# Kernel optimization log

Measured on AMD Instinct MI355X. Metric: run time of the kernel, lower is better.

## Reference

```python
import jax, jax.numpy as jnp
import numpy as np

D = 2048
H = 16
DH = D // H
L = 512  # kv_latent_dim
LN_EPS = 1e-5


def setup_inputs() -> dict:
    key = jax.random.key(0)
    ks = jax.random.split(key, 8)
    s = 0.02  # weight init scale to keep logits in a sane range
    x = jax.random.normal(ks[0], (2, 2048, D), dtype=jnp.float32)
    W_q = jax.random.normal(ks[1], (D, D), dtype=jnp.float32) * s      # torch Linear weight [out,in]
    Wd_kv = jax.random.normal(ks[2], (L, D), dtype=jnp.float32) * s
    W_uv = jax.random.normal(ks[3], (D, L), dtype=jnp.float32) * s
    W_uk = jax.random.normal(ks[4], (D, L), dtype=jnp.float32) * s
    W_o = jax.random.normal(ks[5], (D, D), dtype=jnp.float32) * s
    gamma = jnp.ones((L,), dtype=jnp.float32)
    beta = jnp.zeros((L,), dtype=jnp.float32)
    return {"x": x, "W_q": W_q, "Wd_kv": Wd_kv, "W_uv": W_uv, "W_uk": W_uk,
            "W_o": W_o, "gamma": gamma, "beta": beta}


def _layernorm(h, gamma, beta):
    mu = jnp.mean(h, axis=-1, keepdims=True)
    var = jnp.mean(jnp.square(h - mu), axis=-1, keepdims=True)
    return (h - mu) * jax.lax.rsqrt(var + LN_EPS) * gamma + beta


def reference(x, W_q, Wd_kv, W_uv, W_uk, W_o, gamma, beta):
    B, S, _ = x.shape
    # absorbed K projection: (W_q @ W_uk) -> [H, dh, L]
    absorbed_k = (W_q @ W_uk).reshape(H, DH, L)
    # latent KV: layernorm(x @ Wd_kv^T), [B, S, L]
    c_kv = _layernorm(jnp.einsum('bsd,ld->bsl', x, Wd_kv), gamma, beta)
    S_full = c_kv.shape[1]
    # NOTE: original uses raw x (not W_q(x)) as q; W_q is folded into absorbed_k
    q = x.reshape(B, S, H, DH)
    tmp = jnp.einsum('bshd,hdl->bhsl', q, absorbed_k)              # [B,H,S,L]
    scores = jnp.einsum('bhsl,btl->bhst', tmp, c_kv) / np.sqrt(DH)  # [B,H,S,S_full]
    # causal mask (past_length=0)
    mask = jnp.tril(jnp.ones((S, S_full), dtype=bool), k=0)
    scores = jnp.where(mask[None, None], scores, -jnp.inf)
    attn = jax.nn.softmax(scores, axis=-1)
    v_full = jnp.einsum('btl,dl->btd', c_kv, W_uv).reshape(B, S_full, H, DH)
    ctx = jnp.einsum('bhst,bthd->bshd', attn, v_full).reshape(B, S, D)
    out = jnp.einsum('bsd,od->bso', ctx, W_o)
    return out, c_kv
```

## Files before the change

### kernel.cpp

```cpp
#include <hip/hip_runtime.h>
#include <hip/hip_bf16.h>
#include <cstdint>


typedef __bf16 bf16x8 __attribute__((ext_vector_type(8)));
typedef __bf16 bf16x4 __attribute__((ext_vector_type(4)));
typedef float  f32x4  __attribute__((ext_vector_type(4)));

#define GLOBAL_AS __attribute__((address_space(1)))
#define LDS_AS    __attribute__((address_space(3)))

__device__ __forceinline__ void gload_lds16(const void* g, void* l) {
    __builtin_amdgcn_global_load_lds((const GLOBAL_AS uint32_t*)g,
                                     (LDS_AS uint32_t*)l, 16, 0, 0);
}

__global__ void k_prep(const float* __restrict__ x, const float* __restrict__ wq,
                       const float* __restrict__ wdkv, const float* __restrict__ wuv,
                       const float* __restrict__ wo, const float* __restrict__ wuk,
                       __bf16* __restrict__ xb, __bf16* __restrict__ wqb,
                       __bf16* __restrict__ wdkvb, __bf16* __restrict__ wuvb,
                       __bf16* __restrict__ wob, __bf16* __restrict__ wukT) {
    __shared__ float t[64][65];
    const int bidx = blockIdx.x;
    if (bidx < 9216) {
        long i = (long)bidx * blockDim.x + threadIdx.x;
        const float* src; __bf16* dst; long off;
        if (i < 1048576)      { src = x;    dst = xb;    off = i; }
        else if (i < 1572864) { src = wq;   dst = wqb;   off = i - 1048576; }
        else if (i < 1703936) { src = wdkv; dst = wdkvb; off = i - 1572864; }
        else if (i < 1835008) { src = wuv;  dst = wuvb;  off = i - 1703936; }
        else                  { src = wo;   dst = wob;   off = i - 1835008; }
        long e = off * 8;
        float4 a = *reinterpret_cast<const float4*>(src + e);
        float4 b = *reinterpret_cast<const float4*>(src + e + 4);
        bf16x8 r;
        r[0] = (__bf16)a.x; r[1] = (__bf16)a.y; r[2] = (__bf16)a.z; r[3] = (__bf16)a.w;
        r[4] = (__bf16)b.x; r[5] = (__bf16)b.y; r[6] = (__bf16)b.z; r[7] = (__bf16)b.w;
        *reinterpret_cast<bf16x8*>(dst + e) = r;
    } else {
        const int tb = bidx - 9216;
        const int d0 = (tb & 31) * 64, l0 = (tb >> 5) * 64;
        const int tid = threadIdx.x;
        const int r = tid >> 4, c = (tid & 15) * 4;
        #pragma unroll
        for (int rr = 0; rr < 64; rr += 16) {
            float4 v = *reinterpret_cast<const float4*>(&wuk[(long)(d0 + r + rr) * 512 + l0 + c]);
            t[r + rr][c] = v.x; t[r + rr][c + 1] = v.y;
            t[r + rr][c + 2] = v.z; t[r + rr][c + 3] = v.w;
        }
        __syncthreads();
        const int lr = tid >> 2, dc = (tid & 3) * 16;
        bf16x8 o0, o1;
        #pragma unroll
        for (int i = 0; i < 8; ++i) { o0[i] = (__bf16)t[dc + i][lr]; o1[i] = (__bf16)t[dc + 8 + i][lr]; }
        *reinterpret_cast<bf16x8*>(&wukT[(long)(l0 + lr) * 2048 + d0 + dc]) = o0;
        *reinterpret_cast<bf16x8*>(&wukT[(long)(l0 + lr) * 2048 + d0 + dc + 8]) = o1;
    }
}

__global__ __launch_bounds__(256, 2) void k_gemm_g12(
    const __bf16* __restrict__ Wqb, const __bf16* __restrict__ WukT, __bf16* __restrict__ absk,
    const __bf16* __restrict__ xb, const __bf16* __restrict__ Wdkvb, float* __restrict__ ckvpre,
    float cscale)
{
    __shared__ __bf16 Asm[128][64];
    __shared__ __bf16 Bsm[64][64];
    const int bid = blockIdx.x;
    const bool g1s = (bid < 128);
    const int lbid = g1s ? bid : bid - 128;
    const int tm = (lbid >> 3) * 128, tn = (lbid & 7) * 64;
    const __bf16* A = g1s ? Wqb : xb;
    const __bf16* B = g1s ? WukT : Wdkvb;
    const int tid  = threadIdx.x;
    const int lane = tid & 63, wid = tid >> 6;
    const int r16 = lane & 15, g = lane >> 4;
    const int srow  = lane >> 3;
    const int sslot = lane & 7;
    const int scol  = ((sslot ^ srow) * 8);

    f32x4 acc[2][4];
    #pragma unroll
    for (int m = 0; m < 2; ++m)
        #pragma unroll
        for (int n = 0; n < 4; ++n) acc[m][n] = (f32x4){0.f, 0.f, 0.f, 0.f};

    for (int kt = 0; kt < 2048; kt += 64) {
        __syncthreads();
        #pragma unroll
        for (int c2 = 0; c2 < 4; ++c2) {
            const int chunk = wid * 4 + c2;
            const int row   = chunk * 8 + srow;
            gload_lds16(&A[(long)(tm + row) * 2048 + kt + scol], &Asm[chunk * 8][0]);
        }
        #pragma unroll
        for (int c2 = 0; c2 < 2; ++c2) {
            const int chunk = wid * 2 + c2;
            const int row   = chunk * 8 + srow;
            gload_lds16(&B[(long)(tn + row) * 2048 + kt + scol], &Bsm[chunk * 8][0]);
        }
        __syncthreads();
        #pragma unroll
        for (int kk = 0; kk < 2; ++kk) {
            bf16x8 af[2], bfr[4];
            #pragma unroll
            for (int m = 0; m < 2; ++m) {
                const int row = wid * 32 + m * 16 + r16;
                af[m] = *reinterpret_cast<const bf16x8*>(
                    reinterpret_cast<const char*>(&Asm[0][0]) +
                    row * 128 + (((kk * 4 + g) ^ (row & 7)) * 16));
            }
            #pragma unroll
            for (int n = 0; n < 4; ++n) {
                const int row = n * 16 + r16;
                bfr[n] = *reinterpret_cast<const bf16x8*>(
                    reinterpret_cast<const char*>(&Bsm[0][0]) +
                    row * 128 + (((kk * 4 + g) ^ (row & 7)) * 16));
            }
            #pragma unroll
            for (int m = 0; m < 2; ++m)
                #pragma unroll
                for (int n = 0; n < 4; ++n)
                    acc[m][n] = __builtin_amdgcn_mfma_f32_16x16x32_bf16(af[m], bfr[n], acc[m][n], 0, 0, 0);
        }
    }
    #pragma unroll
    for (int m = 0; m < 2; ++m) {
        #pragma unroll
        for (int n = 0; n < 4; ++n) {
            #pragma unroll
            for (int j = 0; j < 4; ++j) {
                const int row = tm + wid * 32 + m * 16 + g * 4 + j;
                const int col = tn + n * 16 + r16;
                if (g1s) absk[(long)row * 512 + col] = (__bf16)(acc[m][n][j] * cscale);
                else     ckvpre[(long)row * 512 + col] = acc[m][n][j];
            }
        }
    }
}

template <typename CT>
__global__ __launch_bounds__(256, 2) void k_gemm_bt(
    const __bf16* __restrict__ A, const __bf16* __restrict__ B, CT* __restrict__ C,
    int K, int lda, int ldb, int ldc,
    long aOffZ, long bOffZ, long cOffZ, float cmul)
{
    A += (long)blockIdx.z * aOffZ;
    B += (long)blockIdx.z * bOffZ;
    C += (long)blockIdx.z * cOffZ;
    __shared__ __bf16 Asm[128][64];
    __shared__ __bf16 Bsm[128][64];
    const int tid  = threadIdx.x;
    const int lane = tid & 63, wid = tid >> 6;
    const int wr = wid >> 1, wc = wid & 1;
    const int tm = blockIdx.x * 128, tn = blockIdx.y * 128;
    const int r16 = lane & 15, g = lane >> 4;

    const int srow  = lane >> 3;
    const int sslot = lane & 7;
    const int scol  = ((sslot ^ srow) * 8);

    f32x4 acc[4][4];
    #pragma unroll
    for (int m = 0; m < 4; ++m)
        #pragma unroll
        for (int n = 0; n < 4; ++n) acc[m][n] = (f32x4){0.f, 0.f, 0.f, 0.f};

    for (int kt = 0; kt < K; kt += 64) {
        __syncthreads();
        #pragma unroll
        for (int c2 = 0; c2 < 4; ++c2) {
            const int chunk = wid * 4 + c2;
            const int row   = chunk * 8 + srow;
            gload_lds16(&A[(long)(tm + row) * lda + kt + scol], &Asm[chunk * 8][0]);
            gload_lds16(&B[(long)(tn + row) * ldb + kt + scol], &Bsm[chunk * 8][0]);
        }
        __syncthreads();
        #pragma unroll
        for (int kk = 0; kk < 2; ++kk) {
            bf16x8 af[4], bfr[4];
            #pragma unroll
            for (int m = 0; m < 4; ++m) {
                const int row = wr * 64 + m * 16 + r16;
                af[m] = *reinterpret_cast<const bf16x8*>(
                    reinterpret_cast<const char*>(&Asm[0][0]) +
                    row * 128 + (((kk * 4 + g) ^ (row & 7)) * 16));
            }
            #pragma unroll
            for (int n = 0; n < 4; ++n) {
                const int row = wc * 64 + n * 16 + r16;
                bfr[n] = *reinterpret_cast<const bf16x8*>(
                    reinterpret_cast<const char*>(&Bsm[0][0]) +
                    row * 128 + (((kk * 4 + g) ^ (row & 7)) * 16));
            }
            #pragma unroll
            for (int m = 0; m < 4; ++m)
                #pragma unroll
                for (int n = 0; n < 4; ++n)
                    acc[m][n] = __builtin_amdgcn_mfma_f32_16x16x32_bf16(af[m], bfr[n], acc[m][n], 0, 0, 0);
        }
    }
    #pragma unroll
    for (int m = 0; m < 4; ++m) {
        #pragma unroll
        for (int n = 0; n < 4; ++n) {
            #pragma unroll
            for (int j = 0; j < 4; ++j) {
                const int row = tm + wr * 64 + m * 16 + g * 4 + j;
                const int col = tn + wc * 64 + n * 16 + r16;
                C[(long)row * ldc + col] = (CT)(acc[m][n][j] * cmul);
            }
        }
    }
}

__global__ void k_layernorm(const float* __restrict__ pre, const float* __restrict__ gamma,
                            const float* __restrict__ beta, float* __restrict__ out_f32,
                            __bf16* __restrict__ out_bf16) {
    const int row  = blockIdx.x * 4 + (threadIdx.x >> 6);
    const int lane = threadIdx.x & 63;
    const float* p = pre + (long)row * 512;
    float4 v0 = *reinterpret_cast<const float4*>(p + lane * 4);
    float4 v1 = *reinterpret_cast<const float4*>(p + 256 + lane * 4);
    float s  = v0.x + v0.y + v0.z + v0.w + v1.x + v1.y + v1.z + v1.w;
    float s2 = v0.x*v0.x + v0.y*v0.y + v0.z*v0.z + v0.w*v0.w
             + v1.x*v1.x + v1.y*v1.y + v1.z*v1.z + v1.w*v1.w;
    #pragma unroll
    for (int d = 1; d < 64; d <<= 1) { s += __shfl_xor(s, d); s2 += __shfl_xor(s2, d); }
    const float mu  = s * (1.0f / 512.0f);
    const float var = s2 * (1.0f / 512.0f) - mu * mu;
    const float rs  = rsqrtf(var + 1e-5f);
    float4 g0 = *reinterpret_cast<const float4*>(gamma + lane * 4);
    float4 g1 = *reinterpret_cast<const float4*>(gamma + 256 + lane * 4);
    float4 b0 = *reinterpret_cast<const float4*>(beta + lane * 4);
    float4 b1 = *reinterpret_cast<const float4*>(beta + 256 + lane * 4);
    float4 y0, y1;
    y0.x = (v0.x - mu) * rs * g0.x + b0.x;  y0.y = (v0.y - mu) * rs * g0.y + b0.y;
    y0.z = (v0.z - mu) * rs * g0.z + b0.z;  y0.w = (v0.w - mu) * rs * g0.w + b0.w;
    y1.x = (v1.x - mu) * rs * g1.x + b1.x;  y1.y = (v1.y - mu) * rs * g1.y + b1.y;
    y1.z = (v1.z - mu) * rs * g1.z + b1.z;  y1.w = (v1.w - mu) * rs * g1.w + b1.w;
    *reinterpret_cast<float4*>(out_f32 + (long)row * 512 + lane * 4) = y0;
    *reinterpret_cast<float4*>(out_f32 + (long)row * 512 + 256 + lane * 4) = y1;
    bf16x4 z0, z1;
    z0[0] = (__bf16)y0.x; z0[1] = (__bf16)y0.y; z0[2] = (__bf16)y0.z; z0[3] = (__bf16)y0.w;
    z1[0] = (__bf16)y1.x; z1[1] = (__bf16)y1.y; z1[2] = (__bf16)y1.z; z1[3] = (__bf16)y1.w;
    *reinterpret_cast<bf16x4*>(out_bf16 + (long)row * 512 + lane * 4) = z0;
    *reinterpret_cast<bf16x4*>(out_bf16 + (long)row * 512 + 256 + lane * 4) = z1;
}

__global__ __launch_bounds__(256, 2) void k_attn(
    const __bf16* __restrict__ xb,
    const __bf16* __restrict__ Keff,
    const __bf16* __restrict__ vT,
    __bf16* __restrict__ ctx)
{
    __shared__ __bf16 Ks[2][64][128];
    __shared__ __bf16 Vs[2][128][64];
    __shared__ __bf16 Pl[4][16][72];
    const int lane = threadIdx.x & 63;
    const int wid  = threadIdx.x >> 6;
    const int r16  = lane & 15;
    const int g    = lane >> 4;
    const int bid  = blockIdx.x;
    const int gidx = ((bid >> 7) << 3) | (bid & 7);
    const int h = gidx & 15, b = gidx >> 4;
    const int p = (bid >> 3) & 15;
    const int nkt = 32 - p;
    const int qbase[2] = { p * 64 + wid * 16, (31 - p) * 64 + wid * 16 };

    bf16x8 aQ[2][4];
    #pragma unroll
    for (int st = 0; st < 2; ++st) {
        const __bf16* qp = xb + ((long)(b * 2048 + qbase[st] + r16)) * 2048 + h * 128 + g * 8;
        #pragma unroll
        for (int ks = 0; ks < 4; ++ks)
            aQ[st][ks] = *reinterpret_cast<const bf16x8*>(qp + ks * 32);
    }

    f32x4 o[2][8];
    float mrow[2], lrow[2];
    #pragma unroll
    for (int st = 0; st < 2; ++st) {
        #pragma unroll
        for (int d8 = 0; d8 < 8; ++d8) o[st][d8] = (f32x4){0.f, 0.f, 0.f, 0.f};
        mrow[st] = -__builtin_inff(); lrow[st] = 0.f;
    }

    const __bf16* Kb = Keff + (long)h * (4096 * 128) + (long)b * (2048 * 128);
    const __bf16* Vb = vT + (long)h * (128 * 4096) + b * 2048;

    const int ksrow = wid * 4 + (lane >> 4);
    const int kslot = lane & 15;
    const int vsrow = wid * 8 + (lane >> 3);
    const int vslot = lane & 7;

    auto stage = [&](int kt, int buf) {
        const int k0s = kt * 64;
        #pragma unroll
        for (int c = 0; c < 4; ++c) {
            const int row = c * 16 + ksrow;
            const int gcol = ((kslot ^ (row & 15)) << 3);
            gload_lds16(&Kb[(long)(k0s + row) * 128 + gcol], &Ks[buf][c * 16 + wid * 4][0]);
        }
        #pragma unroll
        for (int c = 0; c < 4; ++c) {
            const int row = c * 32 + vsrow;
            const int gcol = ((vslot ^ (row & 7)) << 3);
            gload_lds16(&Vb[(long)row * 4096 + k0s + gcol], &Vs[buf][c * 32 + wid * 8][0]);
        }
    };

    const float THR = 11.541560327f;
    stage(0, 0);
    for (int kt = 0; kt < nkt; ++kt) {
        const int cur = kt & 1;
        const int k0 = kt * 64;
        __syncthreads();
        if (kt + 1 < nkt) stage(kt + 1, cur ^ 1);
        const char* Kbase = reinterpret_cast<const char*>(&Ks[cur][0][0]);
        const char* Vbase = reinterpret_cast<const char*>(&Vs[cur][0][0]);
        const bool light = (kt <= p);

        f32x4 sT[2][4];
        #pragma unroll
        for (int kh = 0; kh < 4; ++kh) {
            sT[0][kh] = (f32x4){0.f, 0.f, 0.f, 0.f};
            sT[1][kh] = (f32x4){0.f, 0.f, 0.f, 0.f};
        }
        __builtin_amdgcn_s_setprio(1);
        #pragma unroll
        for (int kh = 0; kh < 4; ++kh) {
            const int krow = kh * 16 + r16;
            bf16x8 bk[4];
            #pragma unroll
            for (int ks = 0; ks < 4; ++ks)
                bk[ks] = *reinterpret_cast<const bf16x8*>(
                    Kbase + krow * 256 + (((ks * 4 + g) ^ (krow & 15)) * 16));
            #pragma unroll
            for (int ks = 0; ks < 4; ++ks)
                sT[1][kh] = __builtin_amdgcn_mfma_f32_16x16x32_bf16(bk[ks], aQ[1][ks], sT[1][kh], 0, 0, 0);
            if (light) {
                #pragma unroll
                for (int ks = 0; ks < 4; ++ks)
                    sT[0][kh] = __builtin_amdgcn_mfma_f32_16x16x32_bf16(bk[ks], aQ[0][ks], sT[0][kh], 0, 0, 0);
            }
        }
        __builtin_amdgcn_s_setprio(0);

        bf16x8 pa[2][2];
        #pragma unroll
        for (int sti = 0; sti < 2; ++sti) {
            const int st = 1 - sti;
            if (st == 0 && !light) continue;
            const bool diag = (st == 0) ? (kt == p) : (kt == nkt - 1);
            if (diag) {
                const int qabs = qbase[st] + r16;
                #pragma unroll
                for (int kh = 0; kh < 4; ++kh)
                    #pragma unroll
                    for (int j = 0; j < 4; ++j)
                        if (k0 + kh * 16 + g * 4 + j > qabs) sT[st][kh][j] = -1e30f;
            }
            float t01 = fmaxf(sT[st][0][0], sT[st][0][1]), t23 = fmaxf(sT[st][0][2], sT[st][0][3]);
            float t45 = fmaxf(sT[st][1][0], sT[st][1][1]), t67 = fmaxf(sT[st][1][2], sT[st][1][3]);
            float t89 = fmaxf(sT[st][2][0], sT[st][2][1]), tab = fmaxf(sT[st][2][2], sT[st][2][3]);
            float tcd = fmaxf(sT[st][3][0], sT[st][3][1]), tef = fmaxf(sT[st][3][2], sT[st][3][3]);
            float tmax = fmaxf(fmaxf(fmaxf(t01, t23), fmaxf(t45, t67)),
                               fmaxf(fmaxf(t89, tab), fmaxf(tcd, tef)));
            tmax = fmaxf(tmax, __shfl_xor(tmax, 16));
            tmax = fmaxf(tmax, __shfl_xor(tmax, 32));
            const int needi = !__all(tmax <= mrow[st] + THR);
            float m = mrow[st], alpha = 1.f;
            if (needi) {
                const float mnew = fmaxf(m, tmax);
                alpha = __builtin_amdgcn_exp2f(m - mnew);
                m = mnew; mrow[st] = mnew;
            }
            float rsum = 0.f;
            bf16x4 pb[4];
            #pragma unroll
            for (int kh = 0; kh < 4; ++kh) {
                #pragma unroll
                for (int j = 0; j < 4; ++j) {
                    const float pv = __builtin_amdgcn_exp2f(sT[st][kh][j] - m);
                    rsum += pv;
                    pb[kh][j] = (__bf16)pv;
                }
            }
            rsum += __shfl_xor(rsum, 16);
            rsum += __shfl_xor(rsum, 32);
            lrow[st] = lrow[st] * alpha + rsum;
            #pragma unroll
            for (int kh = 0; kh < 4; ++kh)
                *reinterpret_cast<bf16x4*>(&Pl[wid][r16][kh * 16 + g * 4]) = pb[kh];
            pa[st][0] = *reinterpret_cast<const bf16x8*>(&Pl[wid][r16][g * 8]);
            pa[st][1] = *reinterpret_cast<const bf16x8*>(&Pl[wid][r16][32 + g * 8]);
            if (needi) {
                float a4[4];
                #pragma unroll
                for (int j = 0; j < 4; ++j) a4[j] = __shfl(alpha, g * 4 + j);
                #pragma unroll
                for (int d8 = 0; d8 < 8; ++d8) {
                    o[st][d8][0] *= a4[0]; o[st][d8][1] *= a4[1];
                    o[st][d8][2] *= a4[2]; o[st][d8][3] *= a4[3];
                }
            }
        }

        __builtin_amdgcn_s_setprio(1);
        #pragma unroll
        for (int kk = 0; kk < 2; ++kk) {
            #pragma unroll
            for (int d8 = 0; d8 < 8; ++d8) {
                const int vrow = d8 * 16 + r16;
                bf16x8 bv = *reinterpret_cast<const bf16x8*>(
                    Vbase + vrow * 128 + (((kk * 4 + g) ^ (vrow & 7)) * 16));
                o[1][d8] = __builtin_amdgcn_mfma_f32_16x16x32_bf16(pa[1][kk], bv, o[1][d8], 0, 0, 0);
                if (light)
                    o[0][d8] = __builtin_amdgcn_mfma_f32_16x16x32_bf16(pa[0][kk], bv, o[0][d8], 0, 0, 0);
            }
        }
        __builtin_amdgcn_s_setprio(0);
    }
    #pragma unroll
    for (int st = 0; st < 2; ++st) {
        float rl4[4];
        #pragma unroll
        for (int j = 0; j < 4; ++j) rl4[j] = 1.0f / __shfl(lrow[st], g * 4 + j);
        #pragma unroll
        for (int d8 = 0; d8 < 8; ++d8) {
            #pragma unroll
            for (int j = 0; j < 4; ++j) {
                const int row = qbase[st] + g * 4 + j;
                ctx[((long)(b * 2048 + row)) * 2048 + h * 128 + d8 * 16 + r16] =
                    (__bf16)(o[st][d8][j] * rl4[j]);
            }
        }
    }
}

extern "C" void kernel_launch(void* const* d_in, const int* in_sizes, int n_in,
                              void* d_out, int out_size, void* d_ws, size_t ws_size,
                              hipStream_t stream) {
    const float* x     = (const float*)d_in[0];
    const float* W_q   = (const float*)d_in[1];
    const float* Wd_kv = (const float*)d_in[2];
    const float* W_uv  = (const float*)d_in[3];
    const float* W_uk  = (const float*)d_in[4];
    const float* W_o   = (const float*)d_in[5];
    const float* gamma = (const float*)d_in[6];
    const float* beta  = (const float*)d_in[7];
    float* out     = (float*)d_out;
    float* ckv_out = out + 8388608;

    char* ws = (char*)d_ws;
    __bf16* xb     = (__bf16*)(ws + 0);
    __bf16* Wqb    = (__bf16*)(ws + 16777216);
    __bf16* Wdkvb  = (__bf16*)(ws + 25165824);
    __bf16* Wuvb   = (__bf16*)(ws + 27262976);
    __bf16* Wob    = (__bf16*)(ws + 29360128);
    __bf16* WukT   = (__bf16*)(ws + 37748736);
    __bf16* absk   = (__bf16*)(ws + 39845888);
    float*  ckvpre = (float*) (ws + 41943040);
    __bf16* ckvb   = (__bf16*)(ws + 50331648);
    __bf16* Keff   = (__bf16*)(ws + 54525952);
    __bf16* vT     = (__bf16*)(ws + 71303168);
    __bf16* ctx    = (__bf16*)(ws + 88080384);

    k_prep<<<9472, 256, 0, stream>>>(x, W_q, Wd_kv, W_uv, W_o, W_uk,
                                     xb, Wqb, Wdkvb, Wuvb, Wob, WukT);

    const float cscale = 1.4426950408889634f * 0.08838834764831845f;
    k_gemm_g12<<<384, 256, 0, stream>>>(Wqb, WukT, absk, xb, Wdkvb, ckvpre, cscale);
    k_layernorm<<<1024, 256, 0, stream>>>(ckvpre, gamma, beta, ckv_out, ckvb);
    k_gemm_bt<__bf16><<<dim3(32, 1, 16), 256, 0, stream>>>(ckvb, absk, Keff,
        512, 512, 512, 128, 0, 128 * 512, 4096 * 128, 1.0f);
    k_gemm_bt<__bf16><<<dim3(16, 32, 1), 256, 0, stream>>>(Wuvb, ckvb, vT,
        512, 512, 512, 4096, 0, 0, 0, 1.0f);
    k_attn<<<512, 256, 0, stream>>>(xb, Keff, vT, ctx);
    k_gemm_bt<float><<<dim3(32, 16, 1), 256, 0, stream>>>(ctx, Wob, out,
        2048, 2048, 2048, 2048, 0, 0, 0, 1.0f);
}
```

Measured before the change: 193.9 us.

## Give each attention wave 32 query rows using two 64-lane waves per block

The attention kernel now runs 2 waves per block instead of 4. Each wave owns two 16-row query groups, so every K and V fragment read from LDS feeds two MFMAs instead of one. The K/V staging loops are re-indexed so the smaller block still fills the same tiles. This cuts LDS read traffic per MFMA, at the cost of doubled accumulator registers and fewer resident waves per CU to hide latency.

```diff
diff --git a/kernel.cpp b/kernel.cpp
--- a/kernel.cpp
+++ b/kernel.cpp
@@ -248,7 +248,7 @@
     *reinterpret_cast<bf16x4*>(out_bf16 + (long)row * 512 + 256 + lane * 4) = z1;
 }
 
-__global__ __launch_bounds__(256, 2) void k_attn(
+__global__ __launch_bounds__(128, 1) void k_attn(
     const __bf16* __restrict__ xb,
     const __bf16* __restrict__ Keff,
     const __bf16* __restrict__ vT,
@@ -256,7 +256,7 @@
 {
     __shared__ __bf16 Ks[2][64][128];
     __shared__ __bf16 Vs[2][128][64];
-    __shared__ __bf16 Pl[4][16][72];
+    __shared__ __bf16 Pl[2][32][72];
     const int lane = threadIdx.x & 63;
     const int wid  = threadIdx.x >> 6;
     const int r16  = lane & 15;
@@ -266,25 +266,29 @@
     const int h = gidx & 15, b = gidx >> 4;
     const int p = (bid >> 3) & 15;
     const int nkt = 32 - p;
-    const int qbase[2] = { p * 64 + wid * 16, (31 - p) * 64 + wid * 16 };
-
-    bf16x8 aQ[2][4];
-    #pragma unroll
-    for (int st = 0; st < 2; ++st) {
-        const __bf16* qp = xb + ((long)(b * 2048 + qbase[st] + r16)) * 2048 + h * 128 + g * 8;
-        #pragma unroll
-        for (int ks = 0; ks < 4; ++ks)
-            aQ[st][ks] = *reinterpret_cast<const bf16x8*>(qp + ks * 32);
-    }
-
-    f32x4 o[2][8];
-    float mrow[2], lrow[2];
-    #pragma unroll
-    for (int st = 0; st < 2; ++st) {
-        #pragma unroll
-        for (int d8 = 0; d8 < 8; ++d8) o[st][d8] = (f32x4){0.f, 0.f, 0.f, 0.f};
-        mrow[st] = -__builtin_inff(); lrow[st] = 0.f;
-    }
+    const int qbase[2] = { p * 64 + wid * 32, (31 - p) * 64 + wid * 32 };
+
+    bf16x8 aQ[2][2][4];
+    #pragma unroll
+    for (int st = 0; st < 2; ++st)
+        #pragma unroll
+        for (int rg = 0; rg < 2; ++rg) {
+            const __bf16* qp = xb + ((long)(b * 2048 + qbase[st] + rg * 16 + r16)) * 2048 + h * 128 + g * 8;
+            #pragma unroll
+            for (int ks = 0; ks < 4; ++ks)
+                aQ[st][rg][ks] = *reinterpret_cast<const bf16x8*>(qp + ks * 32);
+        }
+
+    f32x4 o[2][2][8];
+    float mrow[2][2], lrow[2][2];
+    #pragma unroll
+    for (int st = 0; st < 2; ++st)
+        #pragma unroll
+        for (int rg = 0; rg < 2; ++rg) {
+            #pragma unroll
+            for (int d8 = 0; d8 < 8; ++d8) o[st][rg][d8] = (f32x4){0.f, 0.f, 0.f, 0.f};
+            mrow[st][rg] = -__builtin_inff(); lrow[st][rg] = 0.f;
+        }
 
     const __bf16* Kb = Keff + (long)h * (4096 * 128) + (long)b * (2048 * 128);
     const __bf16* Vb = vT + (long)h * (128 * 4096) + b * 2048;
@@ -297,16 +301,16 @@
     auto stage = [&](int kt, int buf) {
         const int k0s = kt * 64;
         #pragma unroll
-        for (int c = 0; c < 4; ++c) {
-            const int row = c * 16 + ksrow;
+        for (int c = 0; c < 8; ++c) {
+            const int row = c * 8 + ksrow;
             const int gcol = ((kslot ^ (row & 15)) << 3);
-            gload_lds16(&Kb[(long)(k0s + row) * 128 + gcol], &Ks[buf][c * 16 + wid * 4][0]);
-        }
-        #pragma unroll
-        for (int c = 0; c < 4; ++c) {
-            const int row = c * 32 + vsrow;
+            gload_lds16(&Kb[(long)(k0s + row) * 128 + gcol], &Ks[buf][c * 8 + wid * 4][0]);
+        }
+        #pragma unroll
+        for (int c = 0; c < 8; ++c) {
+            const int row = c * 16 + vsrow;
             const int gcol = ((vslot ^ (row & 7)) << 3);
-            gload_lds16(&Vb[(long)row * 4096 + k0s + gcol], &Vs[buf][c * 32 + wid * 8][0]);
+            gload_lds16(&Vb[(long)row * 4096 + k0s + gcol], &Vs[buf][c * 16 + wid * 8][0]);
         }
     };
 
@@ -321,12 +325,13 @@
         const char* Vbase = reinterpret_cast<const char*>(&Vs[cur][0][0]);
         const bool light = (kt <= p);
 
-        f32x4 sT[2][4];
-        #pragma unroll
-        for (int kh = 0; kh < 4; ++kh) {
-            sT[0][kh] = (f32x4){0.f, 0.f, 0.f, 0.f};
-            sT[1][kh] = (f32x4){0.f, 0.f, 0.f, 0.f};
-        }
+        f32x4 sT[2][2][4];
+        #pragma unroll
+        for (int st = 0; st < 2; ++st)
+            #pragma unroll
+            for (int rg = 0; rg < 2; ++rg)
+                #pragma unroll
+                for (int kh = 0; kh < 4; ++kh) sT[st][rg][kh] = (f32x4){0.f, 0.f, 0.f, 0.f};
         __builtin_amdgcn_s_setprio(1);
         #pragma unroll
         for (int kh = 0; kh < 4; ++kh) {
@@ -337,72 +342,79 @@
                 bk[ks] = *reinterpret_cast<const bf16x8*>(
                     Kbase + krow * 256 + (((ks * 4 + g) ^ (krow & 15)) * 16));
             #pragma unroll
-            for (int ks = 0; ks < 4; ++ks)
-                sT[1][kh] = __builtin_amdgcn_mfma_f32_16x16x32_bf16(bk[ks], aQ[1][ks], sT[1][kh], 0, 0, 0);
+            for (int ks = 0; ks < 4; ++ks) {
+                sT[1][0][kh] = __builtin_amdgcn_mfma_f32_16x16x32_bf16(bk[ks], aQ[1][0][ks], sT[1][0][kh], 0, 0, 0);
+                sT[1][1][kh] = __builtin_amdgcn_mfma_f32_16x16x32_bf16(bk[ks], aQ[1][1][ks], sT[1][1][kh], 0, 0, 0);
+            }
             if (light) {
                 #pragma unroll
-                for (int ks = 0; ks < 4; ++ks)
-                    sT[0][kh] = __builtin_amdgcn_mfma_f32_16x16x32_bf16(bk[ks], aQ[0][ks], sT[0][kh], 0, 0, 0);
+                for (int ks = 0; ks < 4; ++ks) {
+                    sT[0][0][kh] = __builtin_amdgcn_mfma_f32_16x16x32_bf16(bk[ks], aQ[0][0][ks], sT[0][0][kh], 0, 0, 0);
+                    sT[0][1][kh] = __builtin_amdgcn_mfma_f32_16x16x32_bf16(bk[ks], aQ[0][1][ks], sT[0][1][kh], 0, 0, 0);
+                }
             }
         }
         __builtin_amdgcn_s_setprio(0);
 
-        bf16x8 pa[2][2];
+        bf16x8 pa[2][2][2];
         #pragma unroll
         for (int sti = 0; sti < 2; ++sti) {
             const int st = 1 - sti;
             if (st == 0 && !light) continue;
             const bool diag = (st == 0) ? (kt == p) : (kt == nkt - 1);
-            if (diag) {
-                const int qabs = qbase[st] + r16;
+            #pragma unroll
+            for (int rg = 0; rg < 2; ++rg) {
+                if (diag) {
+                    const int qabs = qbase[st] + rg * 16 + r16;
+                    #pragma unroll
+                    for (int kh = 0; kh < 4; ++kh)
+                        #pragma unroll
+                        for (int j = 0; j < 4; ++j)
+                            if (k0 + kh * 16 + g * 4 + j > qabs) sT[st][rg][kh][j] = -1e30f;
+                }
+                float t01 = fmaxf(sT[st][rg][0][0], sT[st][rg][0][1]), t23 = fmaxf(sT[st][rg][0][2], sT[st][rg][0][3]);
+                float t45 = fmaxf(sT[st][rg][1][0], sT[st][rg][1][1]), t67 = fmaxf(sT[st][rg][1][2], sT[st][rg][1][3]);
+                float t89 = fmaxf(sT[st][rg][2][0], sT[st][rg][2][1]), tab = fmaxf(sT[st][rg][2][2], sT[st][rg][2][3]);
+                float tcd = fmaxf(sT[st][rg][3][0], sT[st][rg][3][1]), tef = fmaxf(sT[st][rg][3][2], sT[st][rg][3][3]);
+                float tmax = fmaxf(fmaxf(fmaxf(t01, t23), fmaxf(t45, t67)),
+                                   fmaxf(fmaxf(t89, tab), fmaxf(tcd, tef)));
+                tmax = fmaxf(tmax, __shfl_xor(tmax, 16));
+                tmax = fmaxf(tmax, __shfl_xor(tmax, 32));
+                const int needi = !__all(tmax <= mrow[st][rg] + THR);
+                float m = mrow[st][rg], alpha = 1.f;
+                if (needi) {
+                    const float mnew = fmaxf(m, tmax);
+                    alpha = __builtin_amdgcn_exp2f(m - mnew);
+                    m = mnew; mrow[st][rg] = mnew;
+                }
+                float rsum = 0.f;
+                bf16x4 pb[4];
+                #pragma unroll
+                for (int kh = 0; kh < 4; ++kh) {
+                    #pragma unroll
+                    for (int j = 0; j < 4; ++j) {
+                        const float pv = __builtin_amdgcn_exp2f(sT[st][rg][kh][j] - m);
+                        rsum += pv;
+                        pb[kh][j] = (__bf16)pv;
+                    }
+                }
+                rsum += __shfl_xor(rsum, 16);
+                rsum += __shfl_xor(rsum, 32);
+                lrow[st][rg] = lrow[st][rg] * alpha + rsum;
                 #pragma unroll
                 for (int kh = 0; kh < 4; ++kh)
+                    *reinterpret_cast<bf16x4*>(&Pl[wid][rg * 16 + r16][kh * 16 + g * 4]) = pb[kh];
+                pa[st][rg][0] = *reinterpret_cast<const bf16x8*>(&Pl[wid][rg * 16 + r16][g * 8]);
+                pa[st][rg][1] = *reinterpret_cast<const bf16x8*>(&Pl[wid][rg * 16 + r16][32 + g * 8]);
+                if (needi) {
+                    float a4[4];
                     #pragma unroll
-                    for (int j = 0; j < 4; ++j)
-                        if (k0 + kh * 16 + g * 4 + j > qabs) sT[st][kh][j] = -1e30f;
-            }
-            float t01 = fmaxf(sT[st][0][0], sT[st][0][1]), t23 = fmaxf(sT[st][0][2], sT[st][0][3]);
-            float t45 = fmaxf(sT[st][1][0], sT[st][1][1]), t67 = fmaxf(sT[st][1][2], sT[st][1][3]);
-            float t89 = fmaxf(sT[st][2][0], sT[st][2][1]), tab = fmaxf(sT[st][2][2], sT[st][2][3]);
-            float tcd = fmaxf(sT[st][3][0], sT[st][3][1]), tef = fmaxf(sT[st][3][2], sT[st][3][3]);
-            float tmax = fmaxf(fmaxf(fmaxf(t01, t23), fmaxf(t45, t67)),
-                               fmaxf(fmaxf(t89, tab), fmaxf(tcd, tef)));
-            tmax = fmaxf(tmax, __shfl_xor(tmax, 16));
-            tmax = fmaxf(tmax, __shfl_xor(tmax, 32));
-            const int needi = !__all(tmax <= mrow[st] + THR);
-            float m = mrow[st], alpha = 1.f;
-            if (needi) {
-                const float mnew = fmaxf(m, tmax);
-                alpha = __builtin_amdgcn_exp2f(m - mnew);
-                m = mnew; mrow[st] = mnew;
-            }
-            float rsum = 0.f;
-            bf16x4 pb[4];
-            #pragma unroll
-            for (int kh = 0; kh < 4; ++kh) {
-                #pragma unroll
-                for (int j = 0; j < 4; ++j) {
-                    const float pv = __builtin_amdgcn_exp2f(sT[st][kh][j] - m);
-                    rsum += pv;
-                    pb[kh][j] = (__bf16)pv;
-                }
-            }
-            rsum += __shfl_xor(rsum, 16);
-            rsum += __shfl_xor(rsum, 32);
-            lrow[st] = lrow[st] * alpha + rsum;
-            #pragma unroll
-            for (int kh = 0; kh < 4; ++kh)
-                *reinterpret_cast<bf16x4*>(&Pl[wid][r16][kh * 16 + g * 4]) = pb[kh];
-            pa[st][0] = *reinterpret_cast<const bf16x8*>(&Pl[wid][r16][g * 8]);
-            pa[st][1] = *reinterpret_cast<const bf16x8*>(&Pl[wid][r16][32 + g * 8]);
-            if (needi) {
-                float a4[4];
-                #pragma unroll
-                for (int j = 0; j < 4; ++j) a4[j] = __shfl(alpha, g * 4 + j);
-                #pragma unroll
-                for (int d8 = 0; d8 < 8; ++d8) {
-                    o[st][d8][0] *= a4[0]; o[st][d8][1] *= a4[1];
-                    o[st][d8][2] *= a4[2]; o[st][d8][3] *= a4[3];
+                    for (int j = 0; j < 4; ++j) a4[j] = __shfl(alpha, g * 4 + j);
+                    #pragma unroll
+                    for (int d8 = 0; d8 < 8; ++d8) {
+                        o[st][rg][d8][0] *= a4[0]; o[st][rg][d8][1] *= a4[1];
+                        o[st][rg][d8][2] *= a4[2]; o[st][rg][d8][3] *= a4[3];
+                    }
                 }
             }
         }
@@ -415,25 +427,31 @@
                 const int vrow = d8 * 16 + r16;
                 bf16x8 bv = *reinterpret_cast<const bf16x8*>(
                     Vbase + vrow * 128 + (((kk * 4 + g) ^ (vrow & 7)) * 16));
-                o[1][d8] = __builtin_amdgcn_mfma_f32_16x16x32_bf16(pa[1][kk], bv, o[1][d8], 0, 0, 0);
-                if (light)
-                    o[0][d8] = __builtin_amdgcn_mfma_f32_16x16x32_bf16(pa[0][kk], bv, o[0][d8], 0, 0, 0);
+                o[1][0][d8] = __builtin_amdgcn_mfma_f32_16x16x32_bf16(pa[1][0][kk], bv, o[1][0][d8], 0, 0, 0);
+                o[1][1][d8] = __builtin_amdgcn_mfma_f32_16x16x32_bf16(pa[1][1][kk], bv, o[1][1][d8], 0, 0, 0);
+                if (light) {
+                    o[0][0][d8] = __builtin_amdgcn_mfma_f32_16x16x32_bf16(pa[0][0][kk], bv, o[0][0][d8], 0, 0, 0);
+                    o[0][1][d8] = __builtin_amdgcn_mfma_f32_16x16x32_bf16(pa[0][1][kk], bv, o[0][1][d8], 0, 0, 0);
+                }
             }
         }
         __builtin_amdgcn_s_setprio(0);
     }
     #pragma unroll
     for (int st = 0; st < 2; ++st) {
-        float rl4[4];
-        #pragma unroll
-        for (int j = 0; j < 4; ++j) rl4[j] = 1.0f / __shfl(lrow[st], g * 4 + j);
-        #pragma unroll
-        for (int d8 = 0; d8 < 8; ++d8) {
-            #pragma unroll
-            for (int j = 0; j < 4; ++j) {
-                const int row = qbase[st] + g * 4 + j;
-                ctx[((long)(b * 2048 + row)) * 2048 + h * 128 + d8 * 16 + r16] =
-                    (__bf16)(o[st][d8][j] * rl4[j]);
+        #pragma unroll
+        for (int rg = 0; rg < 2; ++rg) {
+            float rl4[4];
+            #pragma unroll
+            for (int j = 0; j < 4; ++j) rl4[j] = 1.0f / __shfl(lrow[st][rg], g * 4 + j);
+            #pragma unroll
+            for (int d8 = 0; d8 < 8; ++d8) {
+                #pragma unroll
+                for (int j = 0; j < 4; ++j) {
+                    const int row = qbase[st] + rg * 16 + g * 4 + j;
+                    ctx[((long)(b * 2048 + row)) * 2048 + h * 128 + d8 * 16 + r16] =
+                        (__bf16)(o[st][rg][d8][j] * rl4[j]);
+                }
             }
         }
     }
@@ -477,7 +495,7 @@
         512, 512, 512, 128, 0, 128 * 512, 4096 * 128, 1.0f);
     k_gemm_bt<__bf16><<<dim3(16, 32, 1), 256, 0, stream>>>(Wuvb, ckvb, vT,
         512, 512, 512, 4096, 0, 0, 0, 1.0f);
-    k_attn<<<512, 256, 0, stream>>>(xb, Keff, vT, ctx);
+    k_attn<<<512, 128, 0, stream>>>(xb, Keff, vT, ctx);
     k_gemm_bt<float><<<dim3(32, 16, 1), 256, 0, stream>>>(ctx, Wob, out,
         2048, 2048, 2048, 2048, 0, 0, 0, 1.0f);
 }
```

Measured after the change: 241.5 us. +24.6%, slower.
